# Optimization experiments

Measured on AMD Instinct MI355X. Metric: run time of the kernel, lower is better.

Reference implementation:

```python
import jax, jax.numpy as jnp
import numpy as np

N = 50000      # nodes
E = 800000     # edges (avg degree 16)
IN = 128       # in_feats
H = 8          # num_heads
EMB = 32       # attention embedding dim (mode != 'cross')
OUT = 16       # out_feats per head
EF = 7         # edge (bond) feature dim


def setup_inputs() -> dict:
    key = jax.random.key(0)
    ks = jax.random.split(key, 12)
    s = 0.05  # xavier-ish scale
    return {
        "feat": jax.random.normal(ks[0], (N, IN), jnp.float32),
        "bond": jax.random.uniform(ks[1], (E, EF), jnp.float32),
        "src": jax.random.randint(ks[2], (E,), 0, N, jnp.int32),
        "dst": jax.random.randint(ks[3], (E,), 0, N, jnp.int32),
        "Wq": jax.random.normal(ks[4], (IN, H * EMB), jnp.float32) * s,
        "Wk": jax.random.normal(ks[5], (IN, H * EMB), jnp.float32) * s,
        "Wv": jax.random.normal(ks[6], (IN, H * OUT), jnp.float32) * s,
        "Wek": jax.random.normal(ks[7], (EF, H * EMB), jnp.float32) * s,
        "bek": jnp.zeros((H * EMB,), jnp.float32),
        "Wefc": jax.random.normal(ks[8], (EF, H * OUT), jnp.float32) * s,
        "befc": jnp.zeros((H * OUT,), jnp.float32),
        "bias": jnp.zeros((H * OUT,), jnp.float32),
    }


def reference(feat, bond, src, dst, Wq, Wk, Wv, Wek, bek, Wefc, befc, bias):
    n = feat.shape[0]
    # node projections
    q = (feat @ Wq).reshape(n, H, EMB)      # query
    k = (feat @ Wk).reshape(n, H, EMB)      # key
    v = (feat @ Wv).reshape(n, H, OUT)      # ft (values)
    # per-edge key from bond features
    ek = (bond @ Wek + bek).reshape(-1, H, EMB)
    # mode 'add': e = sum((q[u] + k[v]) * edge_key) over embedding dim  -> [E, H]
    e = ((q[src] + k[dst]) * ek).sum(axis=-1)
    # edge_softmax: segment softmax over incoming edges per destination node
    m = jax.ops.segment_max(e, dst, num_segments=n)          # [N, H]
    ex = jnp.exp(e - m[dst])
    denom = jax.ops.segment_sum(ex, dst, num_segments=n)     # [N, H]
    a = ex / denom[dst]                                      # [E, H]
    # per-edge feature projection
    ef = (bond @ Wefc + befc).reshape(-1, H, OUT)
    # message = ft[src] * edge_feat * a, aggregated by sum at dst
    msg = v[src] * ef * a[:, :, None]                        # [E, H, OUT]
    rst = jax.ops.segment_sum(msg, dst, num_segments=n)      # [N, H, OUT]
    rst = rst + bias.reshape(1, H, OUT)
    return rst
```

## Files before the change

kernel.cpp:

```cpp
#include <hip/hip_runtime.h>
#include <hip/hip_bf16.h>

#define HD   8
#define EMBD 32
#define OUTF 16
#define EFD  7
#define INFD 128
#define QKD  256
#define VOD  128
#define GQD  64
#define CAPMAX 64
#define NB   8
#define MAXSLOT 512
#define PBROW 524

typedef __attribute__((ext_vector_type(8))) short short8;
typedef __attribute__((ext_vector_type(4))) float f32x4;

__device__ __forceinline__ float b2f(unsigned short u) {
    return __uint_as_float(((unsigned int)u) << 16);
}
__device__ __forceinline__ unsigned short f2b(float f) {
    __hip_bfloat16 h = __float2bfloat16(f);
    return __builtin_bit_cast(unsigned short, h);
}
__device__ __forceinline__ unsigned short f2h(float f) {
    return __builtin_bit_cast(unsigned short, (_Float16)f);
}
__device__ __forceinline__ float h2f(unsigned short u) {
    return (float)__builtin_bit_cast(_Float16, u);
}

__global__ __launch_bounds__(256) void setup_kernel(
    const float* __restrict__ Wq, const float* __restrict__ Wk,
    const float* __restrict__ Wv, const float* __restrict__ Wek,
    const float* __restrict__ bek, unsigned short* __restrict__ GwT,
    int* __restrict__ counts, int N)
{
    const int b = blockIdx.x, t = threadIdx.x;
    if (b >= 16) {
        int i = (b - 16) * 256 + t;
        int stride = (gridDim.x - 16) * 256;
        for (; i < N; i += stride) counts[i] = 0;
        return;
    }
    if (b >= 8) {
        #pragma unroll
        for (int k = 0; k < 8; k++) {
            int i = (b - 8) * 2048 + k * 256 + t;
            int r = i >> 7, c = i & 127;
            GwT[(size_t)(128 + c) * 128 + r] = f2b(Wv[(size_t)r * VOD + c]);
        }
        return;
    }
    __shared__ float sWek[EFD * QKD];
    __shared__ float sbek[QKD];
    for (int i = t; i < EFD * QKD; i += 256) sWek[i] = Wek[i];
    for (int i = t; i < QKD; i += 256) sbek[i] = bek[i];
    __syncthreads();

    const int p = b * 256 + t;
    const int side = p >> 10;
    const int r = (p >> 3) & 127;
    const int h = p & 7;
    const float* W = side ? Wk : Wq;
    float wrow[EMBD];
    #pragma unroll
    for (int d = 0; d < EMBD; d++) wrow[d] = W[(size_t)r * QKD + h * EMBD + d];
    #pragma unroll
    for (int f = 0; f < EFD; f++) {
        float m = 0.f;
        #pragma unroll
        for (int d = 0; d < EMBD; d++) m += wrow[d] * sWek[f * QKD + h * EMBD + d];
        GwT[(size_t)(side * 64 + h * 8 + f) * 128 + r] = f2b(m);
    }
    float mb = 0.f;
    #pragma unroll
    for (int d = 0; d < EMBD; d++) mb += wrow[d] * sbek[h * EMBD + d];
    GwT[(size_t)(side * 64 + h * 8 + 7) * 128 + r] = f2b(mb);
}

__global__ __launch_bounds__(256) void work_kernel(
    const float* __restrict__ feat, const unsigned short* __restrict__ GwT,
    unsigned short* __restrict__ gq, unsigned short* __restrict__ gk,
    unsigned short* __restrict__ v_bf, int M,
    const int* __restrict__ src, const int* __restrict__ dst,
    const float* __restrict__ bond, int E,
    int* __restrict__ counts, short8* __restrict__ edata, int cap, int pg)
{
    if ((int)blockIdx.x >= pg) {
        int i = (blockIdx.x - pg) * 256 + threadIdx.x;
        int stride = (gridDim.x - pg) * 256;
        for (; i < E; i += stride) {
            int d = dst[i];
            const float* bp = bond + (size_t)i * EFD;
            short8 rec;
            rec[0] = (short)(unsigned short)src[i];
            #pragma unroll
            for (int f = 0; f < EFD; f++) rec[1 + f] = (short)f2b(bp[f]);
            int p = atomicAdd(&counts[d], 1);
            if (p < cap) edata[(size_t)d * cap + p] = rec;
        }
        return;
    }
    const int wave = threadIdx.x >> 6, lane = threadIdx.x & 63;
    const int quad = lane >> 4, l16 = lane & 15;
    const int m0 = blockIdx.x * 64 + wave * 16;
    const int mrow = m0 + l16;
    const int arow = (mrow < M) ? mrow : 0;

    f32x4 acc[16];
    #pragma unroll
    for (int ct = 0; ct < 16; ct++) acc[ct] = (f32x4){0.f, 0.f, 0.f, 0.f};

    #pragma unroll
    for (int ks = 0; ks < 4; ks++) {
        const float* fp = feat + (size_t)arow * INFD + ks * 32 + quad * 8;
        float4 f0 = *(const float4*)(fp);
        float4 f1 = *(const float4*)(fp + 4);
        short8 a;
        a[0] = (short)f2b(f0.x); a[1] = (short)f2b(f0.y);
        a[2] = (short)f2b(f0.z); a[3] = (short)f2b(f0.w);
        a[4] = (short)f2b(f1.x); a[5] = (short)f2b(f1.y);
        a[6] = (short)f2b(f1.z); a[7] = (short)f2b(f1.w);
        #pragma unroll
        for (int ct = 0; ct < 16; ct++) {
            short8 b = *(const short8*)(GwT + (size_t)(ct * 16 + l16) * 128 + ks * 32 + quad * 8);
            acc[ct] = __builtin_amdgcn_mfma_f32_16x16x32_bf16(a, b, acc[ct], 0, 0, 0);
        }
    }

    const int mt = m0 + quad * 4;
    #pragma unroll
    for (int ct = 0; ct < 16; ct++) {
        int nn = ct * 16 + l16;
        unsigned short* outp; int nc, ldo;
        if (ct < 4)      { outp = gq;   nc = nn;       ldo = GQD; }
        else if (ct < 8) { outp = gk;   nc = nn - 64;  ldo = GQD; }
        else             { outp = v_bf; nc = nn - 128; ldo = VOD; }
        #pragma unroll
        for (int r = 0; r < 4; r++) {
            int mm = mt + r;
            if (mm < M) outp[(size_t)mm * ldo + nc] = f2b(acc[ct][r]);
        }
    }
}

__global__ __launch_bounds__(256) void aggregate_kernel(
    const short8* __restrict__ edata,
    const unsigned short* __restrict__ gq,
    const unsigned short* __restrict__ gk,
    const unsigned short* __restrict__ v_bf,
    const int* __restrict__ counts,
    const float* __restrict__ Wefc,
    const float* __restrict__ befc,
    const float* __restrict__ bias,
    float* __restrict__ out, int N, int cap)
{
    __shared__ __align__(16) unsigned short sBond[MAXSLOT][8];
    __shared__ __align__(8)  unsigned short sS[MAXSLOT];
    __shared__ unsigned char sNode[MAXSLOT];
    __shared__ __align__(16) unsigned short sGK[NB * GQD];
    __shared__ __align__(16) unsigned short sPh[8 * PBROW];
    __shared__ float sL[NB * 8];
    __shared__ int sCnt[NB], sR16[NB], sBase[NB], sTot;

    const int t  = threadIdx.x;
    const int n0 = blockIdx.x * NB;
    const int wv = t >> 6;
    const int l  = t & 63;
    const int lrow = l & 15;
    const int lhi  = l >> 4;
    const int c0 = wv * 32 + 2 * lrow;
    const int h0 = c0 >> 4;

    short8 Bfr[2]; float bout[2];
    #pragma unroll
    for (int j = 0; j < 2; j++) {
        short8 b = {0,0,0,0,0,0,0,0};
        float bo = 0.f;
        if (lhi == 0) {
            const int c = c0 + j;
            #pragma unroll
            for (int f = 0; f < EFD; f++) b[f] = (short)f2b(Wefc[f * VOD + c]);
            b[7] = (short)f2b(befc[c]);
            bo = bias[c];
        }
        Bfr[j] = b; bout[j] = bo;
    }

    if (t < 64) {
        int c = 0;
        if (t < NB) {
            int n = n0 + t;
            c = (n < N) ? min(counts[n], cap) : 0;
        }
        int r16 = (c + 15) & ~15;
        int pre = 0;
        #pragma unroll
        for (int j = 0; j < NB; j++) {
            int vj = __shfl(r16, j, 64);
            pre += (j < t) ? vj : 0;
        }
        if (t < NB) {
            sCnt[t] = c; sR16[t] = r16; sBase[t] = pre;
            if (t == NB - 1) sTot = pre + r16;
        }
    }
    {
        const unsigned gi = (unsigned)n0 * 32u + (unsigned)t;
        if (gi < (unsigned)N * 32u)
            ((unsigned*)sGK)[t] = ((const unsigned*)gk)[gi];
    }
    __syncthreads();

    const int tot = sTot;
    {
        const int b1 = sBase[1], b2 = sBase[2], b3 = sBase[3], b4 = sBase[4],
                  b5 = sBase[5], b6 = sBase[6], b7 = sBase[7];
        for (int i = t; i < tot; i += 256) {
            int nn = (i >= b1) + (i >= b2) + (i >= b3) + (i >= b4)
                   + (i >= b5) + (i >= b6) + (i >= b7);
            int el = i - sBase[nn];
            int cnt = sCnt[nn];
            unsigned short sv = 0;
            short8 st = {0,0,0,0,0,0,0,0};
            if (el < cnt) {
                short8 r = edata[(size_t)(n0 + nn) * cap + el];
                sv = (unsigned short)r[0];
                #pragma unroll
                for (int f = 0; f < EFD; f++) st[f] = r[1 + f];
                st[7] = (short)0x3F80;
            }
            sS[i] = sv;
            sNode[i] = (unsigned char)nn;
            *(short8*)&sBond[i][0] = st;
        }
    }
    __syncthreads();

    for (int idx = t; idx < tot * 8; idx += 256) {
        const int sl = idx >> 3, lh = idx & 7;
        short8 bb = *(const short8*)&sBond[sl][0];
        float ex = 0.f;
        if (bb[7]) {
            const int nn = sNode[sl];
            short8 gv = *(const short8*)(gq + (size_t)sS[sl] * GQD + lh * 8);
            short8 kb = *(const short8*)&sGK[nn * GQD + lh * 8];
            float lv = b2f((unsigned short)gv[7]) + b2f((unsigned short)kb[7]);
            #pragma unroll
            for (int f = 0; f < EFD; f++)
                lv += b2f((unsigned short)bb[f]) *
                      (b2f((unsigned short)gv[f]) + b2f((unsigned short)kb[f]));
            ex = __expf(lv);
        }
        sPh[lh * PBROW + sl] = f2h(ex);
    }
    __syncthreads();

    {
        const int nn = t >> 5, h = (t >> 2) & 7, sub = t & 3;
        const int base = sBase[nn], cnt = sCnt[nn];
        float s = 0.f;
        for (int e = sub; e < cnt; e += 4)
            s += h2f(sPh[h * PBROW + base + e]);
        s += __shfl_xor(s, 1, 64);
        s += __shfl_xor(s, 2, 64);
        if (sub == 0) sL[nn * 8 + h] = s;
    }
    __syncthreads();

    for (int nn = 0; nn < NB; nn++) {
        const int n = n0 + nn;
        if (n >= N) break;
        const int r16 = sR16[nn];
        const int sb  = sBase[nn];
        float a0 = 0.f, a1 = 0.f;
        for (int mt = 0; mt < (r16 >> 4); mt++) {
            short8 A = {0,0,0,0,0,0,0,0};
            if (lhi == 0) A = *(const short8*)&sBond[sb + mt * 16 + lrow][0];
            const int e0 = sb + mt * 16 + lhi * 4;
            const unsigned long long sw = *(const unsigned long long*)&sS[e0];
            const unsigned s0 = (unsigned)(sw & 0xffff), s1 = (unsigned)((sw >> 16) & 0xffff);
            const unsigned s2 = (unsigned)((sw >> 32) & 0xffff), s3 = (unsigned)(sw >> 48);
            const unsigned long long pw = *(const unsigned long long*)&sPh[h0 * PBROW + e0];
            const float p0 = h2f((unsigned short)(pw & 0xffff));
            const float p1 = h2f((unsigned short)((pw >> 16) & 0xffff));
            const float p2 = h2f((unsigned short)((pw >> 32) & 0xffff));
            const float p3 = h2f((unsigned short)(pw >> 48));
            const unsigned w0 = *(const unsigned*)(v_bf + s0 * VOD + c0);
            const unsigned w1 = *(const unsigned*)(v_bf + s1 * VOD + c0);
            const unsigned w2 = *(const unsigned*)(v_bf + s2 * VOD + c0);
            const unsigned w3 = *(const unsigned*)(v_bf + s3 * VOD + c0);
            const f32x4 C0 = __builtin_amdgcn_mfma_f32_16x16x32_bf16(
                A, Bfr[0], (f32x4){0.f, 0.f, 0.f, 0.f}, 0, 0, 0);
            const f32x4 C1 = __builtin_amdgcn_mfma_f32_16x16x32_bf16(
                A, Bfr[1], (f32x4){0.f, 0.f, 0.f, 0.f}, 0, 0, 0);
            a0 = fmaf(p0 * C0[0], __uint_as_float(w0 << 16), a0);
            a1 = fmaf(p0 * C1[0], __uint_as_float(w0 & 0xffff0000u), a1);
            a0 = fmaf(p1 * C0[1], __uint_as_float(w1 << 16), a0);
            a1 = fmaf(p1 * C1[1], __uint_as_float(w1 & 0xffff0000u), a1);
            a0 = fmaf(p2 * C0[2], __uint_as_float(w2 << 16), a0);
            a1 = fmaf(p2 * C1[2], __uint_as_float(w2 & 0xffff0000u), a1);
            a0 = fmaf(p3 * C0[3], __uint_as_float(w3 << 16), a0);
            a1 = fmaf(p3 * C1[3], __uint_as_float(w3 & 0xffff0000u), a1);
        }
        a0 += __shfl_xor(a0, 16, 64);
        a0 += __shfl_xor(a0, 32, 64);
        a1 += __shfl_xor(a1, 16, 64);
        a1 += __shfl_xor(a1, 32, 64);
        if (lhi == 0) {
            const float L = sL[nn * 8 + h0];
            const float iv = (L > 0.f) ? 1.f / L : 0.f;
            float2 o;
            o.x = a0 * iv + bout[0];
            o.y = a1 * iv + bout[1];
            *(float2*)&out[(size_t)n * VOD + c0] = o;
        }
    }
}

extern "C" void kernel_launch(void* const* d_in, const int* in_sizes, int n_in,
                              void* d_out, int out_size, void* d_ws, size_t ws_size,
                              hipStream_t stream) {
    const float* feat = (const float*)d_in[0];
    const float* bond = (const float*)d_in[1];
    const int* src  = (const int*)d_in[2];
    const int* dst  = (const int*)d_in[3];
    const float* Wq   = (const float*)d_in[4];
    const float* Wk   = (const float*)d_in[5];
    const float* Wv   = (const float*)d_in[6];
    const float* Wek  = (const float*)d_in[7];
    const float* bek  = (const float*)d_in[8];
    const float* Wefc = (const float*)d_in[9];
    const float* befc = (const float*)d_in[10];
    const float* bias = (const float*)d_in[11];

    const int N = in_sizes[0] / INFD;
    const int E = in_sizes[2];

    size_t off = 0;
    auto carve = [&](size_t bytes) -> void* {
        void* p = (char*)d_ws + off;
        off += (bytes + 255) & ~(size_t)255;
        return p;
    };
    unsigned short* GwT  = (unsigned short*)carve((size_t)256 * 128 * 2);
    unsigned short* gq   = (unsigned short*)carve((size_t)N * GQD * 2);
    unsigned short* gk   = (unsigned short*)carve((size_t)N * GQD * 2);
    unsigned short* v_bf = (unsigned short*)carve((size_t)N * VOD * 2);
    int* counts    = (int*)carve((size_t)N * 4);

    size_t remain = (ws_size > off) ? (ws_size - off) : 0;
    int cap = (int)(remain / ((size_t)N * 16));
    if (cap > 64) cap = 64;
    if (cap > CAPMAX) cap = CAPMAX;
    if (cap < 1) cap = 1;
    short8* edata = (short8*)carve((size_t)N * cap * 16);

    setup_kernel<<<80, 256, 0, stream>>>(Wq, Wk, Wv, Wek, bek, GwT, counts, N);

    const int pg = (N + 63) / 64;
    work_kernel<<<pg + 3072, 256, 0, stream>>>(feat, GwT, gq, gk, v_bf, N,
                                               src, dst, bond, E, counts, edata, cap, pg);

    aggregate_kernel<<<(N + NB - 1) / NB, 256, 0, stream>>>(
        edata, gq, gk, v_bf, counts, Wefc, befc, bias, (float*)d_out, N, cap);
}
```

Measured before the change: 254.2 us.

## Bucket edge indices instead of packed edge records; gather src/bond in aggregate

The scatter phase now writes only a 4-byte edge index per destination slot instead of a 16-byte packed record holding src and bf16 bond features. The aggregate kernel then gathers src and the 7 bond floats from the original arrays through that index. This cuts scatter write traffic and atomic-path work, but moves random gathers of src and bond (28 bytes, uncoalesced) into the aggregate kernel. That kernel was previously reading contiguous per-node records.

Result: slower. 291.6 us (+14.7%).

```diff
diff --git a/kernel.cpp b/kernel.cpp
--- a/kernel.cpp
+++ b/kernel.cpp
@@ -13,6 +13,7 @@
 #define NB   8
 #define MAXSLOT 512
 #define PBROW 524
+#define SCB  3072
 
 typedef __attribute__((ext_vector_type(8))) short short8;
 typedef __attribute__((ext_vector_type(4))) float f32x4;
@@ -84,22 +85,16 @@
     const float* __restrict__ feat, const unsigned short* __restrict__ GwT,
     unsigned short* __restrict__ gq, unsigned short* __restrict__ gk,
     unsigned short* __restrict__ v_bf, int M,
-    const int* __restrict__ src, const int* __restrict__ dst,
-    const float* __restrict__ bond, int E,
-    int* __restrict__ counts, short8* __restrict__ edata, int cap, int pg)
+    const int* __restrict__ dst, int E,
+    int* __restrict__ counts, int* __restrict__ eidx, int cap, int pg)
 {
     if ((int)blockIdx.x >= pg) {
         int i = (blockIdx.x - pg) * 256 + threadIdx.x;
         int stride = (gridDim.x - pg) * 256;
         for (; i < E; i += stride) {
             int d = dst[i];
-            const float* bp = bond + (size_t)i * EFD;
-            short8 rec;
-            rec[0] = (short)(unsigned short)src[i];
-            #pragma unroll
-            for (int f = 0; f < EFD; f++) rec[1 + f] = (short)f2b(bp[f]);
             int p = atomicAdd(&counts[d], 1);
-            if (p < cap) edata[(size_t)d * cap + p] = rec;
+            if (p < cap) eidx[(size_t)d * cap + p] = i;
         }
         return;
     }
@@ -147,7 +142,9 @@
 }
 
 __global__ __launch_bounds__(256) void aggregate_kernel(
-    const short8* __restrict__ edata,
+    const int* __restrict__ eidx,
+    const int* __restrict__ src,
+    const float* __restrict__ bond,
     const unsigned short* __restrict__ gq,
     const unsigned short* __restrict__ gk,
     const unsigned short* __restrict__ v_bf,
@@ -226,10 +223,11 @@
             unsigned short sv = 0;
             short8 st = {0,0,0,0,0,0,0,0};
             if (el < cnt) {
-                short8 r = edata[(size_t)(n0 + nn) * cap + el];
-                sv = (unsigned short)r[0];
+                int eid = eidx[(size_t)(n0 + nn) * cap + el];
+                sv = (unsigned short)src[eid];
+                const float* bp = bond + (size_t)eid * EFD;
                 #pragma unroll
-                for (int f = 0; f < EFD; f++) st[f] = r[1 + f];
+                for (int f = 0; f < EFD; f++) st[f] = (short)f2b(bp[f]);
                 st[7] = (short)0x3F80;
             }
             sS[i] = sv;
@@ -352,18 +350,19 @@
     int* counts    = (int*)carve((size_t)N * 4);
 
     size_t remain = (ws_size > off) ? (ws_size - off) : 0;
-    int cap = (int)(remain / ((size_t)N * 16));
+    int cap = (int)(remain / ((size_t)N * 4));
     if (cap > 64) cap = 64;
     if (cap > CAPMAX) cap = CAPMAX;
     if (cap < 1) cap = 1;
-    short8* edata = (short8*)carve((size_t)N * cap * 16);
+    int* eidx = (int*)carve((size_t)N * cap * 4);
 
     setup_kernel<<<80, 256, 0, stream>>>(Wq, Wk, Wv, Wek, bek, GwT, counts, N);
 
     const int pg = (N + 63) / 64;
-    work_kernel<<<pg + 3072, 256, 0, stream>>>(feat, GwT, gq, gk, v_bf, N,
-                                               src, dst, bond, E, counts, edata, cap, pg);
+    work_kernel<<<pg + SCB, 256, 0, stream>>>(feat, GwT, gq, gk, v_bf, N,
+                                              dst, E, counts, eidx, cap, pg);
 
     aggregate_kernel<<<(N + NB - 1) / NB, 256, 0, stream>>>(
-        edata, gq, gk, v_bf, counts, Wefc, befc, bias, (float*)d_out, N, cap);
-}
+        eidx, src, bond, gq, gk, v_bf, counts, Wefc, befc, bias,
+        (float*)d_out, N, cap);
+}
```
